# Kernel optimization log

Hardware: AMD Instinct MI355X
Metric: run time of the kernel (lower is better)

Reference implementation:

```python
import jax, jax.numpy as jnp
import numpy as np

N, E, L, G, D = 131072, 262144, 16384, 2048, 300
NUM_LAYERS = 5


def setup_inputs() -> dict:
    key = jax.random.key(0)
    ks = jax.random.split(key, 16)
    s = 0.05
    inp = {}
    inp["x"] = jax.random.randint(ks[0], (N, 2), 0, 3, dtype=jnp.int32)
    inp["edge_index"] = jax.random.randint(ks[1], (2, E), 0, N, dtype=jnp.int32)
    inp["edge_attr"] = jax.random.randint(ks[2], (E, 2), 0, 3, dtype=jnp.int32)
    inp["lower_batch"] = jnp.sort(jax.random.randint(ks[3], (N,), 0, L, dtype=jnp.int32))
    inp["upper_batch"] = jnp.sort(jax.random.randint(ks[4], (L,), 0, G, dtype=jnp.int32))
    inp["x_emb1"] = jax.random.normal(ks[5], (120, D), jnp.float32) * s
    inp["x_emb2"] = jax.random.normal(ks[6], (3, D), jnp.float32) * s
    inp["edge_emb1"] = jax.random.normal(ks[7], (NUM_LAYERS, 6, D), jnp.float32) * s
    inp["edge_emb2"] = jax.random.normal(ks[8], (NUM_LAYERS, 3, D), jnp.float32) * s
    inp["mlp_w1"] = jax.random.normal(ks[9], (NUM_LAYERS, D, 2 * D), jnp.float32) * s
    inp["mlp_b1"] = jnp.zeros((NUM_LAYERS, 2 * D), jnp.float32)
    inp["mlp_w2"] = jax.random.normal(ks[10], (NUM_LAYERS, 2 * D, D), jnp.float32) * s
    inp["mlp_b2"] = jnp.zeros((NUM_LAYERS, D), jnp.float32)
    inp["bn_gamma"] = jnp.ones((NUM_LAYERS, D), jnp.float32)
    inp["bn_beta"] = jnp.zeros((NUM_LAYERS, D), jnp.float32)
    inp["cls_w1"] = jax.random.normal(ks[11], (D, D), jnp.float32) * s
    inp["cls_b1"] = jnp.zeros((D,), jnp.float32)
    inp["cls_w2"] = jax.random.normal(ks[12], (D, 1), jnp.float32) * s
    inp["cls_b2"] = jnp.zeros((1,), jnp.float32)
    return inp


def _segment_mean(data, seg, num):
    s = jax.ops.segment_sum(data, seg, num_segments=num)
    c = jax.ops.segment_sum(jnp.ones((data.shape[0], 1), data.dtype), seg, num_segments=num)
    return s / jnp.maximum(c, 1.0)


def reference(x, edge_index, edge_attr, lower_batch, upper_batch,
              x_emb1, x_emb2, edge_emb1, edge_emb2,
              mlp_w1, mlp_b1, mlp_w2, mlp_b2, bn_gamma, bn_beta,
              cls_w1, cls_b1, cls_w2, cls_b2):
    eps = 1e-5
    # node embeddings
    h = x_emb1[x[:, 0]] + x_emb2[x[:, 1]]  # [N, D]
    # add self loops with edge_attr (4, 0)
    loop = jnp.arange(N, dtype=edge_index.dtype)
    src = jnp.concatenate([edge_index[0], loop])
    dst = jnp.concatenate([edge_index[1], loop])
    ea0 = jnp.concatenate([edge_attr[:, 0], jnp.full((N,), 4, edge_attr.dtype)])
    ea1 = jnp.concatenate([edge_attr[:, 1], jnp.zeros((N,), edge_attr.dtype)])
    for l in range(NUM_LAYERS):
        e = edge_emb1[l][ea0] + edge_emb2[l][ea1]        # [E+N, D]
        msg = h[src] + e                                  # gather + add
        agg = jax.ops.segment_sum(msg, dst, num_segments=N)  # scatter-add
        h2 = jax.nn.relu(agg @ mlp_w1[l] + mlp_b1[l]) @ mlp_w2[l] + mlp_b2[l]
        # BatchNorm1d (training mode, biased var)
        mu = jnp.mean(h2, axis=0)
        var = jnp.var(h2, axis=0)
        h2 = (h2 - mu) * jax.lax.rsqrt(var + eps) * bn_gamma[l] + bn_beta[l]
        h = h2 if l == NUM_LAYERS - 1 else jax.nn.relu(h2)
    # hierarchical pooling: node -> lower substructure (mean), lower -> graph (mean)
    lower = _segment_mean(h, lower_batch, L)  # [L, D]

    def classify(feat):
        pooled = _segment_mean(feat, upper_batch, G)  # [G, D]
        hh = jax.nn.relu(pooled @ cls_w1 + cls_b1)
        return (hh @ cls_w2 + cls_b2)[:, 0]

    logits0 = classify(lower)
    logits1 = classify(jnp.roll(lower, 1, axis=0))  # aug_type == 'roll'
    return jnp.concatenate([logits0, logits1])  # [2G]
```

## Files before the change

kernel.cpp:

```cpp
#include <hip/hip_runtime.h>

#define N_NODES 131072
#define E_EDGES 262144
#define L_SEG 16384
#define G_SEG 2048
#define D_FEAT 300
#define NUM_LAYERS 5
#define MCHUNK 65536
#define HS 304
#define KP1 320
#define KP2 608
#define NP1 640
#define NP2 384

typedef unsigned short u16;
typedef unsigned int u32;
typedef __attribute__((ext_vector_type(8))) short short8v;
typedef __attribute__((ext_vector_type(4))) float f32x4;

struct __align__(16) U128 { u32 a, b, c, d; };
struct __align__(8) U64 { u32 a, b; };

__device__ __forceinline__ float bf2f(u16 u) { return __uint_as_float(((u32)u) << 16); }
__device__ __forceinline__ u16 f2bf(float f) {
  u32 x = __float_as_uint(f);
  x += 0x7fffu + ((x >> 16) & 1u);
  return (u16)(x >> 16);
}
__device__ __forceinline__ u32 pack2(float x, float y) {
  return (u32)f2bf(x) | ((u32)f2bf(y) << 16);
}

__device__ __forceinline__ void gl2lds16(const void* g, void* l) {
  auto gp = reinterpret_cast<const __attribute__((address_space(1))) void*>(
      reinterpret_cast<uintptr_t>(g));
  auto lp = reinterpret_cast<__attribute__((address_space(3))) void*>(
      reinterpret_cast<uintptr_t>(l));
  __builtin_amdgcn_global_load_lds(gp, lp, 16, 0, 0);
}

__global__ void k_init_h(const int* __restrict__ x, const float* __restrict__ e1,
                         const float* __restrict__ e2, u16* __restrict__ h) {
  int i = blockIdx.x * blockDim.x + threadIdx.x;
  if (i >= N_NODES * 76) return;
  int n = i / 76, q = i - n * 76;
  int col = q * 4;
  ushort4 o = make_ushort4(0, 0, 0, 0);
  if (col < 300) {
    int x0 = x[2 * n], x1 = x[2 * n + 1];
    float4 va = *(const float4*)(e1 + (size_t)x0 * D_FEAT + col);
    float4 vb = *(const float4*)(e2 + (size_t)x1 * D_FEAT + col);
    o.x = f2bf(va.x + vb.x); o.y = f2bf(va.y + vb.y);
    o.z = f2bf(va.z + vb.z); o.w = f2bf(va.w + vb.w);
  }
  *(ushort4*)(h + (size_t)n * HS + col) = o;
}

__global__ void k_prepw(const float* __restrict__ w, u16* __restrict__ wt,
                        int K, int Ncol, int NP, int KP) {
  int l = blockIdx.y;
  int i = blockIdx.x * blockDim.x + threadIdx.x;
  if (i >= NP * KP) return;
  int n = i / KP, k = i - n * KP;
  float v = (n < Ncol && k < K) ? w[(size_t)l * K * Ncol + (size_t)k * Ncol + n] : 0.f;
  wt[(size_t)l * NP * KP + i] = f2bf(v);
}

__global__ void k_zero(float* __restrict__ p, int n) {
  int i = blockIdx.x * blockDim.x + threadIdx.x;
  if (i < n) p[i] = 0.f;
}
__global__ void k_hist(const int* __restrict__ ei, int* __restrict__ cnt) {
  int e = blockIdx.x * blockDim.x + threadIdx.x;
  if (e < E_EDGES) atomicAdd(&cnt[ei[E_EDGES + e]], 1);
}
__global__ __launch_bounds__(1024) void k_scan(const int* __restrict__ cnt,
                                               int* __restrict__ offs,
                                               int* __restrict__ cursor) {
  __shared__ int part[1024];
  int t = threadIdx.x;
  int base = t * 128;
  int s = 0;
  for (int i = 0; i < 128; i++) s += cnt[base + i];
  part[t] = s;
  __syncthreads();
  for (int off = 1; off < 1024; off <<= 1) {
    int v = (t >= off) ? part[t - off] : 0;
    __syncthreads();
    part[t] += v;
    __syncthreads();
  }
  int run = (t == 0) ? 0 : part[t - 1];
  for (int i = 0; i < 128; i++) {
    offs[base + i] = run;
    cursor[base + i] = run;
    run += cnt[base + i];
  }
  if (t == 1023) offs[N_NODES] = run;
}
__global__ void k_fill(const int* __restrict__ ei, int* __restrict__ cursor,
                       int* __restrict__ elist) {
  int e = blockIdx.x * blockDim.x + threadIdx.x;
  if (e < E_EDGES) {
    int p = atomicAdd(&cursor[ei[E_EDGES + e]], 1);
    elist[p] = e;
  }
}

__global__ void k_gather(const u32* __restrict__ h, const int* __restrict__ ei,
                         const int* __restrict__ ea, const int* __restrict__ offs,
                         const int* __restrict__ elist, const float* __restrict__ sc1,
                         const float* __restrict__ sc2, const float* __restrict__ ee1,
                         const float* __restrict__ ee2, u32* __restrict__ agg) {
  int n = (blockIdx.x << 2) + (threadIdx.x >> 6);
  int lane = threadIdx.x & 63;
  int j0 = lane, j1 = lane + 64, j2 = lane + 128;
  float ax0, ay0, ax1, ay1, ax2 = 0.f, ay2 = 0.f;
  const u32* hn = h + (size_t)n * (HS / 2);
  {
    u32 u = hn[j0];
    ax0 = bf2f((u16)(u & 0xffffu)) + sc1[2 * j0] + sc2[2 * j0];
    ay0 = bf2f((u16)(u >> 16)) + sc1[2 * j0 + 1] + sc2[2 * j0 + 1];
    u = hn[j1];
    ax1 = bf2f((u16)(u & 0xffffu)) + sc1[2 * j1] + sc2[2 * j1];
    ay1 = bf2f((u16)(u >> 16)) + sc1[2 * j1 + 1] + sc2[2 * j1 + 1];
    if (j2 < 150) {
      u = hn[j2];
      ax2 = bf2f((u16)(u & 0xffffu)) + sc1[2 * j2] + sc2[2 * j2];
      ay2 = bf2f((u16)(u >> 16)) + sc1[2 * j2 + 1] + sc2[2 * j2 + 1];
    }
  }
  int p = offs[n], pe = offs[n + 1];
  while (p + 2 <= pe) {
    int eA = elist[p], eB = elist[p + 1];
    int sA = ei[eA], sB = ei[eB];
    int a0A = ea[2 * eA], a1A = ea[2 * eA + 1];
    int a0B = ea[2 * eB], a1B = ea[2 * eB + 1];
    const u32* hA = h + (size_t)sA * (HS / 2);
    const u32* hB = h + (size_t)sB * (HS / 2);
    const float* p1A = ee1 + (size_t)a0A * D_FEAT;
    const float* p2A = ee2 + (size_t)a1A * D_FEAT;
    const float* p1B = ee1 + (size_t)a0B * D_FEAT;
    const float* p2B = ee2 + (size_t)a1B * D_FEAT;
    u32 uA0 = hA[j0], uA1 = hA[j1];
    u32 uB0 = hB[j0], uB1 = hB[j1];
    u32 uA2 = 0, uB2 = 0;
    if (j2 < 150) { uA2 = hA[j2]; uB2 = hB[j2]; }
    ax0 += bf2f((u16)(uA0 & 0xffffu)) + p1A[2 * j0] + p2A[2 * j0];
    ay0 += bf2f((u16)(uA0 >> 16)) + p1A[2 * j0 + 1] + p2A[2 * j0 + 1];
    ax1 += bf2f((u16)(uA1 & 0xffffu)) + p1A[2 * j1] + p2A[2 * j1];
    ay1 += bf2f((u16)(uA1 >> 16)) + p1A[2 * j1 + 1] + p2A[2 * j1 + 1];
    if (j2 < 150) {
      ax2 += bf2f((u16)(uA2 & 0xffffu)) + p1A[2 * j2] + p2A[2 * j2];
      ay2 += bf2f((u16)(uA2 >> 16)) + p1A[2 * j2 + 1] + p2A[2 * j2 + 1];
    }
    ax0 += bf2f((u16)(uB0 & 0xffffu)) + p1B[2 * j0] + p2B[2 * j0];
    ay0 += bf2f((u16)(uB0 >> 16)) + p1B[2 * j0 + 1] + p2B[2 * j0 + 1];
    ax1 += bf2f((u16)(uB1 & 0xffffu)) + p1B[2 * j1] + p2B[2 * j1];
    ay1 += bf2f((u16)(uB1 >> 16)) + p1B[2 * j1 + 1] + p2B[2 * j1 + 1];
    if (j2 < 150) {
      ax2 += bf2f((u16)(uB2 & 0xffffu)) + p1B[2 * j2] + p2B[2 * j2];
      ay2 += bf2f((u16)(uB2 >> 16)) + p1B[2 * j2 + 1] + p2B[2 * j2 + 1];
    }
    p += 2;
  }
  if (p < pe) {
    int e = elist[p];
    int s = ei[e];
    int a0 = ea[2 * e], a1 = ea[2 * e + 1];
    const u32* hs = h + (size_t)s * (HS / 2);
    const float* p1 = ee1 + (size_t)a0 * D_FEAT;
    const float* p2 = ee2 + (size_t)a1 * D_FEAT;
    u32 u = hs[j0];
    ax0 += bf2f((u16)(u & 0xffffu)) + p1[2 * j0] + p2[2 * j0];
    ay0 += bf2f((u16)(u >> 16)) + p1[2 * j0 + 1] + p2[2 * j0 + 1];
    u = hs[j1];
    ax1 += bf2f((u16)(u & 0xffffu)) + p1[2 * j1] + p2[2 * j1];
    ay1 += bf2f((u16)(u >> 16)) + p1[2 * j1 + 1] + p2[2 * j1 + 1];
    if (j2 < 150) {
      u = hs[j2];
      ax2 += bf2f((u16)(u & 0xffffu)) + p1[2 * j2] + p2[2 * j2];
      ay2 += bf2f((u16)(u >> 16)) + p1[2 * j2 + 1] + p2[2 * j2 + 1];
    }
  }
  u32* ao = agg + (size_t)n * (KP1 / 2);
  ao[j0] = pack2(ax0, ay0);
  ao[j1] = pack2(ax1, ay1);
  if (j2 < 150) ao[j2] = pack2(ax2, ay2);
  else if (j2 < 160) ao[j2] = 0u;
}

template <bool RELU, int KP>
__global__ __launch_bounds__(512) void k_gemm_mfma(const u16* __restrict__ A,
                                                   const u16* __restrict__ WT,
                                                   const float* __restrict__ bias,
                                                   u16* __restrict__ C, int Ncol,
                                                   int Cstride, float* __restrict__ stats) {
  __shared__ __align__(16) u16 SL[24576];
  int t = threadIdx.x;
  int w = t >> 6, lane = t & 63;
  int brow = blockIdx.y << 8, bcol = blockIdx.x << 7;
  int wr = w >> 1, wc = w & 1;
  int r16 = lane & 15, kq = lane >> 4;
  int rq = kq << 2;

  f32x4 zero4 = {0.f, 0.f, 0.f, 0.f};
  f32x4 acc[4][4];
#pragma unroll
  for (int mi = 0; mi < 4; mi++)
#pragma unroll
    for (int nj = 0; nj < 4; nj++) acc[mi][nj] = zero4;

  int m0 = 2 * w, m1 = m0 + 1;
  const u16* gA0 = A + (size_t)(brow + m0 * 16 + r16) * KP + kq * 8;
  const u16* gA1 = A + (size_t)(brow + m1 * 16 + r16) * KP + kq * 8;
  const u16* gB = WT + (size_t)(bcol + w * 16 + r16) * KP + kq * 8;

  gl2lds16(gA0, SL + m0 * 512);
  gl2lds16(gA1, SL + m1 * 512);
  gl2lds16(gB, SL + 8192 + w * 512);
  __syncthreads();

  int cur = 0;
  for (int k0 = 0; k0 < KP; k0 += 32) {
    u16* curb = SL + cur * 12288;
    u16* nxtb = SL + (cur ^ 1) * 12288;
    if (k0 + 32 < KP) {
      gl2lds16(gA0 + k0 + 32, nxtb + m0 * 512);
      gl2lds16(gA1 + k0 + 32, nxtb + m1 * 512);
      gl2lds16(gB + k0 + 32, nxtb + 8192 + w * 512);
    }
    short8v af[4], bf[4];
#pragma unroll
    for (int mi = 0; mi < 4; mi++)
      af[mi] = *(const short8v*)(curb + (wr * 4 + mi) * 512 + lane * 8);
#pragma unroll
    for (int nj = 0; nj < 4; nj++)
      bf[nj] = *(const short8v*)(curb + 8192 + (wc * 4 + nj) * 512 + lane * 8);
#pragma unroll
    for (int mi = 0; mi < 4; mi++)
#pragma unroll
      for (int nj = 0; nj < 4; nj++)
        acc[mi][nj] = __builtin_amdgcn_mfma_f32_16x16x32_bf16(af[mi], bf[nj], acc[mi][nj], 0, 0, 0);
    __syncthreads();
    cur ^= 1;
  }

#pragma unroll
  for (int p = 0; p < 4; p++) {
    if (wr == p) {
#pragma unroll
      for (int nj = 0; nj < 4; nj++) {
        int col = wc * 64 + nj * 16 + r16;
        int gcol = bcol + col;
        bool live = gcol < Ncol;
        float bs = live ? bias[gcol] : 0.f;
#pragma unroll
        for (int mi = 0; mi < 4; mi++) {
#pragma unroll
          for (int j = 0; j < 4; j++) {
            float v = acc[mi][nj][j] + bs;
            if (RELU) v = fmaxf(v, 0.f);
            if (!live) v = 0.f;
            SL[(mi * 16 + rq + j) * 132 + col] = f2bf(v);
          }
        }
      }
    }
    __syncthreads();
    {
      int r = t >> 3, s = t & 7;
      size_t grow = (size_t)(brow + p * 64 + r) * Cstride;
#pragma unroll
      for (int c = 0; c < 2; c++) {
        int colu = s * 16 + c * 8;
        int gcol = bcol + colu;
        if (gcol + 8 <= Cstride) {
          U64 v0 = *(const U64*)(SL + r * 132 + colu);
          U64 v1 = *(const U64*)(SL + r * 132 + colu + 4);
          *(U64*)(C + grow + gcol) = v0;
          *(U64*)(C + grow + gcol + 4) = v1;
        }
      }
    }
    if (stats != nullptr && t < 128) {
      int gcol = bcol + t;
      if (gcol < Ncol) {
        float s0 = 0.f, q0 = 0.f;
#pragma unroll 8
        for (int r = 0; r < 64; r++) {
          float v = bf2f(SL[r * 132 + t]);
          s0 += v;
          q0 = fmaf(v, v, q0);
        }
        atomicAdd(stats + gcol, s0);
        atomicAdd(stats + 304 + gcol, q0);
      }
    }
    __syncthreads();
  }
}

__global__ void k_bnfin(const float* __restrict__ sums, const float* __restrict__ gamma,
                        const float* __restrict__ beta, float* __restrict__ fa,
                        float* __restrict__ fc) {
  int d = blockIdx.x * blockDim.x + threadIdx.x;
  if (d >= HS) return;
  float a = 0.f, c = 0.f;
  if (d < D_FEAT) {
    const float inv = 1.f / (float)N_NODES;
    float mu = sums[d] * inv;
    float var = sums[304 + d] * inv - mu * mu;
    a = rsqrtf(var + 1e-5f) * gamma[d];
    c = beta[d] - mu * a;
  }
  fa[d] = a;
  fc[d] = c;
}

__global__ void k_bnnorm(u16* __restrict__ h, const float* __restrict__ fa,
                         const float* __restrict__ fc, int relu) {
  int i = blockIdx.x * blockDim.x + threadIdx.x;
  if (i >= N_NODES * 38) return;
  int n = i / 38, q = i - n * 38;
  int col = q * 8;
  u16* hp = h + (size_t)n * HS + col;
  float4 a0 = *(const float4*)(fa + col);
  float4 a1 = *(const float4*)(fa + col + 4);
  float4 c0 = *(const float4*)(fc + col);
  float4 c1 = *(const float4*)(fc + col + 4);
  ushort4 u0 = *(ushort4*)hp;
  ushort4 u1 = *(ushort4*)(hp + 4);
  float r0, r1, r2, r3, r4, r5, r6, r7;
#define BN1(res, uv, A, C)                       \
  res = fmaf((A), bf2f(uv), (C));                \
  if (relu) res = fmaxf(res, 0.f);
  BN1(r0, u0.x, a0.x, c0.x) BN1(r1, u0.y, a0.y, c0.y)
  BN1(r2, u0.z, a0.z, c0.z) BN1(r3, u0.w, a0.w, c0.w)
  BN1(r4, u1.x, a1.x, c1.x) BN1(r5, u1.y, a1.y, c1.y)
  BN1(r6, u1.z, a1.z, c1.z) BN1(r7, u1.w, a1.w, c1.w)
#undef BN1
  ushort4 o0, o1;
  o0.x = f2bf(r0); o0.y = f2bf(r1); o0.z = f2bf(r2); o0.w = f2bf(r3);
  o1.x = f2bf(r4); o1.y = f2bf(r5); o1.z = f2bf(r6); o1.w = f2bf(r7);
  *(ushort4*)hp = o0;
  *(ushort4*)(hp + 4) = o1;
}

__device__ __forceinline__ int lowerBound(const int* __restrict__ a, int n, int v) {
  int lo = 0, hi = n;
  while (lo < hi) {
    int m = (lo + hi) >> 1;
    if (a[m] < v) lo = m + 1; else hi = m;
  }
  return lo;
}

__global__ void k_lower(const u16* __restrict__ h, const int* __restrict__ lb,
                        float* __restrict__ lower) {
  int g = blockIdx.x;
  int s = lowerBound(lb, N_NODES, g);
  int e = lowerBound(lb, N_NODES, g + 1);
  float invc = 1.f / (float)max(e - s, 1);
  for (int d = threadIdx.x; d < D_FEAT; d += 256) {
    float acc = 0.f;
    for (int r = s; r < e; r++) acc += bf2f(h[(size_t)r * HS + d]);
    lower[(size_t)g * D_FEAT + d] = acc * invc;
  }
}

__global__ void k_pooled(const float* __restrict__ lower, const int* __restrict__ ub,
                         float* __restrict__ pooled) {
  int g = blockIdx.x, br = blockIdx.y;
  int s = lowerBound(ub, L_SEG, g);
  int e = lowerBound(ub, L_SEG, g + 1);
  float invc = 1.f / (float)max(e - s, 1);
  for (int d = threadIdx.x; d < D_FEAT; d += 256) {
    float acc = 0.f;
    for (int i = s; i < e; i++) {
      int row = br ? (i - 1 + L_SEG) % L_SEG : i;
      acc += lower[(size_t)row * D_FEAT + d];
    }
    pooled[((size_t)br * G_SEG + g) * D_FEAT + d] = acc * invc;
  }
}

__global__ __launch_bounds__(256) void k_classify(const float* __restrict__ pooled,
                                                  const float* __restrict__ w1,
                                                  const float* __restrict__ b1,
                                                  const float* __restrict__ w2,
                                                  const float* __restrict__ b2,
                                                  float* __restrict__ out) {
  __shared__ float p[D_FEAT];
  __shared__ float red[4];
  int g = blockIdx.x, br = blockIdx.y;
  const float* pr = pooled + ((size_t)br * G_SEG + g) * D_FEAT;
  for (int d = threadIdx.x; d < D_FEAT; d += 256) p[d] = pr[d];
  __syncthreads();
  float partial = 0.f;
  for (int j = threadIdx.x; j < D_FEAT; j += 256) {
    float acc = b1[j];
    for (int k = 0; k < D_FEAT; k++) acc = fmaf(p[k], w1[(size_t)k * D_FEAT + j], acc);
    acc = fmaxf(acc, 0.f);
    partial += acc * w2[j];
  }
  for (int off = 32; off; off >>= 1) partial += __shfl_down(partial, off, 64);
  int lane = threadIdx.x & 63, wid = threadIdx.x >> 6;
  if (lane == 0) red[wid] = partial;
  __syncthreads();
  if (threadIdx.x == 0) out[(size_t)br * G_SEG + g] = red[0] + red[1] + red[2] + red[3] + b2[0];
}

extern "C" void kernel_launch(void* const* d_in, const int* in_sizes, int n_in,
                              void* d_out, int out_size, void* d_ws, size_t ws_size,
                              hipStream_t stream) {
  const int* x = (const int*)d_in[0];
  const int* ei = (const int*)d_in[1];
  const int* ea = (const int*)d_in[2];
  const int* lb = (const int*)d_in[3];
  const int* ub = (const int*)d_in[4];
  const float* xe1 = (const float*)d_in[5];
  const float* xe2 = (const float*)d_in[6];
  const float* ee1 = (const float*)d_in[7];
  const float* ee2 = (const float*)d_in[8];
  const float* w1 = (const float*)d_in[9];
  const float* b1 = (const float*)d_in[10];
  const float* w2 = (const float*)d_in[11];
  const float* b2 = (const float*)d_in[12];
  const float* gam = (const float*)d_in[13];
  const float* bet = (const float*)d_in[14];
  const float* cw1 = (const float*)d_in[15];
  const float* cb1 = (const float*)d_in[16];
  const float* cw2 = (const float*)d_in[17];
  const float* cb2 = (const float*)d_in[18];
  float* out = (float*)d_out;

  char* base = (char*)d_ws;
  size_t off = 0;
  auto alloc = [&](size_t bytes) -> void* {
    void* p = base + off;
    off += (bytes + 255) & ~(size_t)255;
    return p;
  };
  u16* h = (u16*)alloc((size_t)N_NODES * HS * 2);
  u16* agg = (u16*)alloc((size_t)N_NODES * KP1 * 2);
  u16* tbuf = (u16*)alloc((size_t)MCHUNK * KP2 * 2);
  u16* W1T = (u16*)alloc((size_t)NUM_LAYERS * NP1 * KP1 * 2);
  u16* W2T = (u16*)alloc((size_t)NUM_LAYERS * NP2 * KP2 * 2);
  int* cnt = (int*)alloc((size_t)N_NODES * 4);
  int* offs = (int*)alloc((size_t)(N_NODES + 1) * 4);
  int* cursor = (int*)alloc((size_t)N_NODES * 4);
  int* elist = (int*)alloc((size_t)E_EDGES * 4);
  float* stats = (float*)alloc(608 * 4);
  float* aff_a = (float*)alloc(HS * 4);
  float* aff_c = (float*)alloc(HS * 4);
  float* lower = (float*)tbuf;
  float* pooled = lower + (size_t)L_SEG * D_FEAT;

  if (ws_size < off) {
    k_zero<<<(out_size + 255) / 256, 256, 0, stream>>>(out, out_size);
    return;
  }

  const int NT = 256;

  k_prepw<<<dim3((NP1 * KP1 + NT - 1) / NT, NUM_LAYERS), NT, 0, stream>>>(w1, W1T, 300, 600, NP1, KP1);
  k_prepw<<<dim3((NP2 * KP2 + NT - 1) / NT, NUM_LAYERS), NT, 0, stream>>>(w2, W2T, 600, 300, NP2, KP2);

  k_zero<<<(N_NODES + NT - 1) / NT, NT, 0, stream>>>((float*)cnt, N_NODES);
  k_hist<<<(E_EDGES + NT - 1) / NT, NT, 0, stream>>>(ei, cnt);
  k_scan<<<1, 1024, 0, stream>>>(cnt, offs, cursor);
  k_fill<<<(E_EDGES + NT - 1) / NT, NT, 0, stream>>>(ei, cursor, elist);

  k_init_h<<<(N_NODES * 76 + NT - 1) / NT, NT, 0, stream>>>(x, xe1, xe2, h);

  for (int l = 0; l < NUM_LAYERS; l++) {
    k_gather<<<N_NODES / 4, NT, 0, stream>>>(
        (const u32*)h, ei, ea, offs, elist,
        ee1 + ((size_t)l * 6 + 4) * D_FEAT, ee2 + (size_t)l * 3 * D_FEAT,
        ee1 + (size_t)l * 6 * D_FEAT, ee2 + (size_t)l * 3 * D_FEAT, (u32*)agg);
    k_zero<<<3, NT, 0, stream>>>(stats, 608);
    for (int c0 = 0; c0 < N_NODES; c0 += MCHUNK) {
      dim3 g1(5, MCHUNK / 256);
      k_gemm_mfma<true, KP1><<<g1, 512, 0, stream>>>(
          agg + (size_t)c0 * KP1, W1T + (size_t)l * NP1 * KP1, b1 + (size_t)l * 600,
          tbuf, 600, KP2, nullptr);
      dim3 g2(3, MCHUNK / 256);
      k_gemm_mfma<false, KP2><<<g2, 512, 0, stream>>>(
          tbuf, W2T + (size_t)l * NP2 * KP2, b2 + (size_t)l * 300,
          h + (size_t)c0 * HS, 300, HS, stats);
    }
    k_bnfin<<<2, NT, 0, stream>>>(stats, gam + (size_t)l * 300, bet + (size_t)l * 300,
                                  aff_a, aff_c);
    k_bnnorm<<<(N_NODES * 38 + NT - 1) / NT, NT, 0, stream>>>(
        h, aff_a, aff_c, l < NUM_LAYERS - 1 ? 1 : 0);
  }

  k_lower<<<L_SEG, NT, 0, stream>>>(h, lb, lower);
  dim3 gp(G_SEG, 2);
  k_pooled<<<gp, NT, 0, stream>>>(lower, ub, pooled);
  k_classify<<<gp, NT, 0, stream>>>(pooled, cw1, cb1, cw2, cb2, out);
}
```

Baseline: 2.443 ms.

## Triple-buffer GEMM LDS tiles with explicit vmcnt waits and one barrier per step

Moves the MFMA GEMM's K-loop from double-buffered LDS staging with two __syncthreads per iteration to a three-stage ring buffer. Loads are issued two steps ahead, and each step waits with s_waitcnt vmcnt(3) before a single s_barrier. The goal is to hide global-to-LDS latency better and cut barrier stalls. In exchange, LDS use per block grows by 50% (72 KB), which may lower occupancy, and correctness now depends on the exact count of outstanding loads per wave.

```diff
diff --git a/kernel.cpp b/kernel.cpp
--- a/kernel.cpp
+++ b/kernel.cpp
@@ -196,7 +196,7 @@
                                                    const float* __restrict__ bias,
                                                    u16* __restrict__ C, int Ncol,
                                                    int Cstride, float* __restrict__ stats) {
-  __shared__ __align__(16) u16 SL[24576];
+  __shared__ __align__(16) u16 SL[36864];
   int t = threadIdx.x;
   int w = t >> 6, lane = t & 63;
   int brow = blockIdx.y << 8, bcol = blockIdx.x << 7;
@@ -219,17 +219,31 @@
   gl2lds16(gA0, SL + m0 * 512);
   gl2lds16(gA1, SL + m1 * 512);
   gl2lds16(gB, SL + 8192 + w * 512);
-  __syncthreads();
-
-  int cur = 0;
+  if (KP > 32) {
+    gl2lds16(gA0 + 32, SL + 12288 + m0 * 512);
+    gl2lds16(gA1 + 32, SL + 12288 + m1 * 512);
+    gl2lds16(gB + 32, SL + 12288 + 8192 + w * 512);
+  }
+
+  int bi = 0;
   for (int k0 = 0; k0 < KP; k0 += 32) {
-    u16* curb = SL + cur * 12288;
-    u16* nxtb = SL + (cur ^ 1) * 12288;
     if (k0 + 32 < KP) {
-      gl2lds16(gA0 + k0 + 32, nxtb + m0 * 512);
-      gl2lds16(gA1 + k0 + 32, nxtb + m1 * 512);
-      gl2lds16(gB + k0 + 32, nxtb + 8192 + w * 512);
-    }
+      asm volatile("s_waitcnt vmcnt(3)" ::: "memory");
+    } else {
+      asm volatile("s_waitcnt vmcnt(0)" ::: "memory");
+    }
+    __builtin_amdgcn_sched_barrier(0);
+    __builtin_amdgcn_s_barrier();
+    __builtin_amdgcn_sched_barrier(0);
+    if (k0 + 64 < KP) {
+      int nb = bi + 2;
+      nb = (nb >= 3) ? nb - 3 : nb;
+      u16* nxtb = SL + nb * 12288;
+      gl2lds16(gA0 + k0 + 64, nxtb + m0 * 512);
+      gl2lds16(gA1 + k0 + 64, nxtb + m1 * 512);
+      gl2lds16(gB + k0 + 64, nxtb + 8192 + w * 512);
+    }
+    u16* curb = SL + bi * 12288;
     short8v af[4], bf[4];
 #pragma unroll
     for (int mi = 0; mi < 4; mi++)
@@ -242,9 +256,10 @@
 #pragma unroll
       for (int nj = 0; nj < 4; nj++)
         acc[mi][nj] = __builtin_amdgcn_mfma_f32_16x16x32_bf16(af[mi], bf[nj], acc[mi][nj], 0, 0, 0);
-    __syncthreads();
-    cur ^= 1;
-  }
+    bi = (bi == 2) ? 0 : bi + 1;
+  }
+  __builtin_amdgcn_sched_barrier(0);
+  __syncthreads();
 
 #pragma unroll
   for (int p = 0; p < 4; p++) {
@@ -258,11 +273,11 @@
 #pragma unroll
         for (int mi = 0; mi < 4; mi++) {
 #pragma unroll
-          for (int j = 0; j < 4; j++) {
-            float v = acc[mi][nj][j] + bs;
+          for (int jj = 0; jj < 4; jj++) {
+            float v = acc[mi][nj][jj] + bs;
             if (RELU) v = fmaxf(v, 0.f);
             if (!live) v = 0.f;
-            SL[(mi * 16 + rq + j) * 132 + col] = f2bf(v);
+            SL[(mi * 16 + rq + jj) * 132 + col] = f2bf(v);
           }
         }
       }
```

New measurement: 2.260 ms. 7.5% less time.

## Fuse both MLP GEMMs into one kernel keeping the hidden tile in LDS

Applied to the files above, without the earlier changes.

Replaces the two chunked MFMA GEMM launches per layer with a single fused kernel. Each 64-row block computes the first GEMM plus ReLU, writes the 600-wide hidden activations straight to shared memory in MFMA fragment order, then runs the second GEMM from LDS and writes h plus the BatchNorm statistics. Weights are pre-packed into fragment-contiguous blocks and read directly from global/L2, not staged in LDS. This removes the global round trip for the intermediate buffer, at the cost of a large LDS footprint and many accumulator registers, which lowers occupancy and drops the double-buffered global-to-LDS prefetch.

```diff
diff --git a/kernel.cpp b/kernel.cpp
--- a/kernel.cpp
+++ b/kernel.cpp
@@ -6,12 +6,13 @@
 #define G_SEG 2048
 #define D_FEAT 300
 #define NUM_LAYERS 5
-#define MCHUNK 65536
 #define HS 304
 #define KP1 320
 #define KP2 608
-#define NP1 640
-#define NP2 384
+#define NB1 40
+#define NK1 10
+#define NB2 24
+#define NK2 19
 
 typedef unsigned short u16;
 typedef unsigned int u32;
@@ -29,14 +30,6 @@
 }
 __device__ __forceinline__ u32 pack2(float x, float y) {
   return (u32)f2bf(x) | ((u32)f2bf(y) << 16);
-}
-
-__device__ __forceinline__ void gl2lds16(const void* g, void* l) {
-  auto gp = reinterpret_cast<const __attribute__((address_space(1))) void*>(
-      reinterpret_cast<uintptr_t>(g));
-  auto lp = reinterpret_cast<__attribute__((address_space(3))) void*>(
-      reinterpret_cast<uintptr_t>(l));
-  __builtin_amdgcn_global_load_lds(gp, lp, 16, 0, 0);
 }
 
 __global__ void k_init_h(const int* __restrict__ x, const float* __restrict__ e1,
@@ -56,14 +49,21 @@
   *(ushort4*)(h + (size_t)n * HS + col) = o;
 }
 
-__global__ void k_prepw(const float* __restrict__ w, u16* __restrict__ wt,
-                        int K, int Ncol, int NP, int KP) {
+__global__ void k_packw(const float* __restrict__ w, u16* __restrict__ wp,
+                        int K, int Ncol, int NB, int NK) {
   int l = blockIdx.y;
   int i = blockIdx.x * blockDim.x + threadIdx.x;
-  if (i >= NP * KP) return;
-  int n = i / KP, k = i - n * KP;
+  int tot = NB * NK * 512;
+  if (i >= tot) return;
+  int nb = i / (NK * 512);
+  int r = i - nb * (NK * 512);
+  int ks = r / 512;
+  int s = r - ks * 512;
+  int lane2 = s >> 3, c = s & 7;
+  int n = nb * 16 + (lane2 & 15);
+  int k = ks * 32 + (lane2 >> 4) * 8 + c;
   float v = (n < Ncol && k < K) ? w[(size_t)l * K * Ncol + (size_t)k * Ncol + n] : 0.f;
-  wt[(size_t)l * NP * KP + i] = f2bf(v);
+  wp[(size_t)l * tot + i] = f2bf(v);
 }
 
 __global__ void k_zero(float* __restrict__ p, int n) {
@@ -190,114 +190,114 @@
   else if (j2 < 160) ao[j2] = 0u;
 }
 
-template <bool RELU, int KP>
-__global__ __launch_bounds__(512) void k_gemm_mfma(const u16* __restrict__ A,
-                                                   const u16* __restrict__ WT,
-                                                   const float* __restrict__ bias,
-                                                   u16* __restrict__ C, int Ncol,
-                                                   int Cstride, float* __restrict__ stats) {
-  __shared__ __align__(16) u16 SL[24576];
+__global__ __launch_bounds__(512) void k_mlp(const u16* __restrict__ agg,
+                                             const u16* __restrict__ W1P,
+                                             const float* __restrict__ b1,
+                                             const u16* __restrict__ W2P,
+                                             const float* __restrict__ b2,
+                                             u16* __restrict__ h,
+                                             float* __restrict__ stats) {
+  __shared__ __align__(16) u16 TL[4 * NK2 * 512];
   int t = threadIdx.x;
   int w = t >> 6, lane = t & 63;
-  int brow = blockIdx.y << 8, bcol = blockIdx.x << 7;
-  int wr = w >> 1, wc = w & 1;
-  int r16 = lane & 15, kq = lane >> 4;
-  int rq = kq << 2;
+  int wr = w >> 2, wc = w & 3;
+  int r16 = lane & 15, kq = lane >> 4, rq = kq << 2;
+  int brow = blockIdx.x << 6;
 
   f32x4 zero4 = {0.f, 0.f, 0.f, 0.f};
-  f32x4 acc[4][4];
-#pragma unroll
-  for (int mi = 0; mi < 4; mi++)
-#pragma unroll
-    for (int nj = 0; nj < 4; nj++) acc[mi][nj] = zero4;
-
-  int m0 = 2 * w, m1 = m0 + 1;
-  const u16* gA0 = A + (size_t)(brow + m0 * 16 + r16) * KP + kq * 8;
-  const u16* gA1 = A + (size_t)(brow + m1 * 16 + r16) * KP + kq * 8;
-  const u16* gB = WT + (size_t)(bcol + w * 16 + r16) * KP + kq * 8;
-
-  gl2lds16(gA0, SL + m0 * 512);
-  gl2lds16(gA1, SL + m1 * 512);
-  gl2lds16(gB, SL + 8192 + w * 512);
-  __syncthreads();
-
-  int cur = 0;
-  for (int k0 = 0; k0 < KP; k0 += 32) {
-    u16* curb = SL + cur * 12288;
-    u16* nxtb = SL + (cur ^ 1) * 12288;
-    if (k0 + 32 < KP) {
-      gl2lds16(gA0 + k0 + 32, nxtb + m0 * 512);
-      gl2lds16(gA1 + k0 + 32, nxtb + m1 * 512);
-      gl2lds16(gB + k0 + 32, nxtb + 8192 + w * 512);
-    }
-    short8v af[4], bf[4];
-#pragma unroll
-    for (int mi = 0; mi < 4; mi++)
-      af[mi] = *(const short8v*)(curb + (wr * 4 + mi) * 512 + lane * 8);
-#pragma unroll
-    for (int nj = 0; nj < 4; nj++)
-      bf[nj] = *(const short8v*)(curb + 8192 + (wc * 4 + nj) * 512 + lane * 8);
-#pragma unroll
-    for (int mi = 0; mi < 4; mi++)
-#pragma unroll
-      for (int nj = 0; nj < 4; nj++)
-        acc[mi][nj] = __builtin_amdgcn_mfma_f32_16x16x32_bf16(af[mi], bf[nj], acc[mi][nj], 0, 0, 0);
-    __syncthreads();
-    cur ^= 1;
-  }
-
-#pragma unroll
-  for (int p = 0; p < 4; p++) {
-    if (wr == p) {
-#pragma unroll
-      for (int nj = 0; nj < 4; nj++) {
-        int col = wc * 64 + nj * 16 + r16;
-        int gcol = bcol + col;
-        bool live = gcol < Ncol;
-        float bs = live ? bias[gcol] : 0.f;
-#pragma unroll
-        for (int mi = 0; mi < 4; mi++) {
-#pragma unroll
-          for (int j = 0; j < 4; j++) {
-            float v = acc[mi][nj][j] + bs;
-            if (RELU) v = fmaxf(v, 0.f);
-            if (!live) v = 0.f;
-            SL[(mi * 16 + rq + j) * 132 + col] = f2bf(v);
-          }
+
+  f32x4 acc1[2][10];
+#pragma unroll
+  for (int fr = 0; fr < 2; fr++)
+#pragma unroll
+    for (int fc = 0; fc < 10; fc++) acc1[fr][fc] = zero4;
+
+  const u16* Ab = agg + (size_t)(brow + wr * 32 + r16) * KP1 + kq * 8;
+  const u16* W1w = W1P + (size_t)(wc * 10) * NK1 * 512 + lane * 8;
+  for (int ks = 0; ks < NK1; ks++) {
+    short8v af0 = *(const short8v*)(Ab + ks * 32);
+    short8v af1 = *(const short8v*)(Ab + 16 * KP1 + ks * 32);
+#pragma unroll
+    for (int fc = 0; fc < 10; fc++) {
+      short8v bf = *(const short8v*)(W1w + (size_t)(fc * NK1 + ks) * 512);
+      acc1[0][fc] = __builtin_amdgcn_mfma_f32_16x16x32_bf16(af0, bf, acc1[0][fc], 0, 0, 0);
+      acc1[1][fc] = __builtin_amdgcn_mfma_f32_16x16x32_bf16(af1, bf, acc1[1][fc], 0, 0, 0);
+    }
+  }
+
+#pragma unroll
+  for (int fc = 0; fc < 10; fc++) {
+    int col = wc * 160 + fc * 16 + r16;
+    if (col < KP2) {
+      float bs = (col < 600) ? b1[col] : 0.f;
+      int ks2 = wc * 5 + (fc >> 1);
+      int coff = (((fc & 1) * 2 + (r16 >> 3)) * 16) * 8 + (r16 & 7);
+#pragma unroll
+      for (int fr = 0; fr < 2; fr++) {
+        u16* blk = TL + (size_t)((wr * 2 + fr) * NK2 + ks2) * 512;
+#pragma unroll
+        for (int j = 0; j < 4; j++) {
+          float v = fmaxf(acc1[fr][fc][j] + bs, 0.f);
+          blk[coff + (rq + j) * 8] = f2bf(v);
         }
       }
     }
-    __syncthreads();
-    {
-      int r = t >> 3, s = t & 7;
-      size_t grow = (size_t)(brow + p * 64 + r) * Cstride;
-#pragma unroll
-      for (int c = 0; c < 2; c++) {
-        int colu = s * 16 + c * 8;
-        int gcol = bcol + colu;
-        if (gcol + 8 <= Cstride) {
-          U64 v0 = *(const U64*)(SL + r * 132 + colu);
-          U64 v1 = *(const U64*)(SL + r * 132 + colu + 4);
-          *(U64*)(C + grow + gcol) = v0;
-          *(U64*)(C + grow + gcol + 4) = v1;
-        }
+  }
+  __syncthreads();
+
+  f32x4 acc2[2][6];
+#pragma unroll
+  for (int fr = 0; fr < 2; fr++)
+#pragma unroll
+    for (int fc = 0; fc < 6; fc++) acc2[fr][fc] = zero4;
+
+  const u16* W2w = W2P + (size_t)(wc * 6) * NK2 * 512 + lane * 8;
+  for (int ks = 0; ks < NK2; ks++) {
+    short8v af0 = *(const short8v*)(TL + (size_t)((wr * 2 + 0) * NK2 + ks) * 512 + lane * 8);
+    short8v af1 = *(const short8v*)(TL + (size_t)((wr * 2 + 1) * NK2 + ks) * 512 + lane * 8);
+#pragma unroll
+    for (int fc = 0; fc < 6; fc++) {
+      short8v bf = *(const short8v*)(W2w + (size_t)(fc * NK2 + ks) * 512);
+      acc2[0][fc] = __builtin_amdgcn_mfma_f32_16x16x32_bf16(af0, bf, acc2[0][fc], 0, 0, 0);
+      acc2[1][fc] = __builtin_amdgcn_mfma_f32_16x16x32_bf16(af1, bf, acc2[1][fc], 0, 0, 0);
+    }
+  }
+  __syncthreads();
+
+  u16* HT = TL;
+#pragma unroll
+  for (int fc = 0; fc < 6; fc++) {
+    int col = wc * 96 + fc * 16 + r16;
+    bool live = col < 300;
+    float bs = live ? b2[col] : 0.f;
+#pragma unroll
+    for (int fr = 0; fr < 2; fr++) {
+      int row = wr * 32 + fr * 16 + rq;
+#pragma unroll
+      for (int j = 0; j < 4; j++) {
+        float v = acc2[fr][fc][j] + bs;
+        if (!live) v = 0.f;
+        HT[(size_t)(row + j) * 392 + col] = f2bf(v);
       }
     }
-    if (stats != nullptr && t < 128) {
-      int gcol = bcol + t;
-      if (gcol < Ncol) {
-        float s0 = 0.f, q0 = 0.f;
+  }
+  __syncthreads();
+
+  for (int i = t; i < 64 * 38; i += 512) {
+    int r = i / 38, c8 = (i - r * 38) * 8;
+    U128 v = *(const U128*)(HT + (size_t)r * 392 + c8);
+    *(U128*)(h + (size_t)(brow + r) * HS + c8) = v;
+  }
+  if (t < 300) {
+    float s0 = 0.f, q0 = 0.f;
 #pragma unroll 8
-        for (int r = 0; r < 64; r++) {
-          float v = bf2f(SL[r * 132 + t]);
-          s0 += v;
-          q0 = fmaf(v, v, q0);
-        }
-        atomicAdd(stats + gcol, s0);
-        atomicAdd(stats + 304 + gcol, q0);
-      }
-    }
-    __syncthreads();
+    for (int r = 0; r < 64; r++) {
+      float v = bf2f(HT[(size_t)r * 392 + t]);
+      s0 += v;
+      q0 = fmaf(v, v, q0);
+    }
+    atomicAdd(stats + t, s0);
+    atomicAdd(stats + 304 + t, q0);
   }
 }
 
@@ -444,9 +444,8 @@
   };
   u16* h = (u16*)alloc((size_t)N_NODES * HS * 2);
   u16* agg = (u16*)alloc((size_t)N_NODES * KP1 * 2);
-  u16* tbuf = (u16*)alloc((size_t)MCHUNK * KP2 * 2);
-  u16* W1T = (u16*)alloc((size_t)NUM_LAYERS * NP1 * KP1 * 2);
-  u16* W2T = (u16*)alloc((size_t)NUM_LAYERS * NP2 * KP2 * 2);
+  u16* W1P = (u16*)alloc((size_t)NUM_LAYERS * NB1 * NK1 * 512 * 2);
+  u16* W2P = (u16*)alloc((size_t)NUM_LAYERS * NB2 * NK2 * 512 * 2);
   int* cnt = (int*)alloc((size_t)N_NODES * 4);
   int* offs = (int*)alloc((size_t)(N_NODES + 1) * 4);
   int* cursor = (int*)alloc((size_t)N_NODES * 4);
@@ -454,7 +453,7 @@
   float* stats = (float*)alloc(608 * 4);
   float* aff_a = (float*)alloc(HS * 4);
   float* aff_c = (float*)alloc(HS * 4);
-  float* lower = (float*)tbuf;
+  float* lower = (float*)agg;
   float* pooled = lower + (size_t)L_SEG * D_FEAT;
 
   if (ws_size < off) {
@@ -464,8 +463,10 @@
 
   const int NT = 256;
 
-  k_prepw<<<dim3((NP1 * KP1 + NT - 1) / NT, NUM_LAYERS), NT, 0, stream>>>(w1, W1T, 300, 600, NP1, KP1);
-  k_prepw<<<dim3((NP2 * KP2 + NT - 1) / NT, NUM_LAYERS), NT, 0, stream>>>(w2, W2T, 600, 300, NP2, KP2);
+  k_packw<<<dim3((NB1 * NK1 * 512 + NT - 1) / NT, NUM_LAYERS), NT, 0, stream>>>(
+      w1, W1P, 300, 600, NB1, NK1);
+  k_packw<<<dim3((NB2 * NK2 * 512 + NT - 1) / NT, NUM_LAYERS), NT, 0, stream>>>(
+      w2, W2P, 600, 300, NB2, NK2);
 
   k_zero<<<(N_NODES + NT - 1) / NT, NT, 0, stream>>>((float*)cnt, N_NODES);
   k_hist<<<(E_EDGES + NT - 1) / NT, NT, 0, stream>>>(ei, cnt);
@@ -480,16 +481,9 @@
         ee1 + ((size_t)l * 6 + 4) * D_FEAT, ee2 + (size_t)l * 3 * D_FEAT,
         ee1 + (size_t)l * 6 * D_FEAT, ee2 + (size_t)l * 3 * D_FEAT, (u32*)agg);
     k_zero<<<3, NT, 0, stream>>>(stats, 608);
-    for (int c0 = 0; c0 < N_NODES; c0 += MCHUNK) {
-      dim3 g1(5, MCHUNK / 256);
-      k_gemm_mfma<true, KP1><<<g1, 512, 0, stream>>>(
-          agg + (size_t)c0 * KP1, W1T + (size_t)l * NP1 * KP1, b1 + (size_t)l * 600,
-          tbuf, 600, KP2, nullptr);
-      dim3 g2(3, MCHUNK / 256);
-      k_gemm_mfma<false, KP2><<<g2, 512, 0, stream>>>(
-          tbuf, W2T + (size_t)l * NP2 * KP2, b2 + (size_t)l * 300,
-          h + (size_t)c0 * HS, 300, HS, stats);
-    }
+    k_mlp<<<N_NODES / 64, 512, 0, stream>>>(
+        agg, W1P + (size_t)l * NB1 * NK1 * 512, b1 + (size_t)l * 600,
+        W2P + (size_t)l * NB2 * NK2 * 512, b2 + (size_t)l * 300, h, stats);
     k_bnfin<<<2, NT, 0, stream>>>(stats, gam + (size_t)l * 300, bet + (size_t)l * 300,
                                   aff_a, aff_c);
     k_bnnorm<<<(N_NODES * 38 + NT - 1) / NT, NT, 0, stream>>>(
```

After: 2.245 ms. -8.1%, faster.
